# Kernel optimization log

Hardware: AMD Instinct MI355X
Metric: run time of the kernel (lower is better)

Reference implementation:

```python
import jax, jax.numpy as jnp
import numpy as np

B, S, D, H = 2, 2048, 1024, 16
HEAD_DIM = D // H
SCALE = HEAD_DIM ** -0.5


def setup_inputs() -> dict:
    key = jax.random.key(0)
    k1, k2, k3 = jax.random.split(key, 3)
    x = jax.random.normal(k1, (B, S, D), dtype=jnp.float32)
    # torch nn.Linear convention: weight is [out_features, in_features], y = x @ W.T + b
    W_qkv = jax.random.normal(k2, (3 * D, D), dtype=jnp.float32) * 0.02  # qkv Linear, bias=False
    W_out = jax.random.normal(k3, (D, D), dtype=jnp.float32) * 0.02
    b_out = jnp.zeros((D,), dtype=jnp.float32)
    return {"x": x, "W_qkv": W_qkv, "W_out": W_out, "b_out": b_out}


def reference(x, W_qkv, W_out, b_out):
    b, s, d_model = x.shape
    # qkv projection (no bias), then split 'b c (qkv h d) -> qkv b h c d'
    qkv = (x @ W_qkv.T).reshape(b, s, 3, H, HEAD_DIM).transpose(2, 0, 3, 1, 4)
    q, k, v = qkv[0], qkv[1], qkv[2]  # each [b, h, s, hd]
    # naive full attention: scores materialized as [b, h, s, s]
    attn = jax.nn.softmax(jnp.einsum('bhxd,bhyd->bhxy', q, k) * SCALE, axis=-1)
    # dropout is identity (rate 0 / eval mode)
    o = jnp.einsum('bhxy,bhyd->bhxd', attn, v)
    o = o.transpose(0, 2, 1, 3).reshape(b, s, d_model)  # 'b h c d -> b c (h d)'
    return o @ W_out.T + b_out
```

## Files before the change

### kernel.cpp

```cpp
#include <hip/hip_runtime.h>


typedef __attribute__((ext_vector_type(8))) short short8;
typedef __attribute__((ext_vector_type(4))) float f32x4;
typedef unsigned short ushort_t;
typedef unsigned int uint32;

#define AS1 __attribute__((address_space(1)))
#define AS3 __attribute__((address_space(3)))

__device__ __forceinline__ void gload_lds16(const void* gp, void* lp) {
    __builtin_amdgcn_global_load_lds((const AS1 void*)gp, (AS3 void*)lp, 16, 0, 0);
}

#if __has_builtin(__builtin_amdgcn_exp2f)
#define EXP2F(x) __builtin_amdgcn_exp2f(x)
#else
#define EXP2F(x) exp2f(x)
#endif

__device__ __forceinline__ uint32 rhu(float f) { return __float_as_uint(f) + 0x8000u; }
#if __has_builtin(__builtin_amdgcn_perm)
__device__ __forceinline__ uint32 pk2bf(float a, float b) {
    return __builtin_amdgcn_perm(rhu(b), rhu(a), 0x07060302u);
}
#else
__device__ __forceinline__ uint32 pk2bf(float a, float b) {
    return (rhu(a) >> 16) | (rhu(b) & 0xffff0000u);
}
#endif
__device__ __forceinline__ ushort_t f2bf(float f) { return (ushort_t)(rhu(f) >> 16); }

__global__ void cvt_all(const float* __restrict__ x, ushort_t* __restrict__ xb,
                        const float* __restrict__ wq, ushort_t* __restrict__ wqb,
                        const float* __restrict__ wo, ushort_t* __restrict__ wob) {
    int blk = blockIdx.x;
    const float* in; ushort_t* out;
    if (blk < 4096)      { in = x;  out = xb;  }
    else if (blk < 7168) { in = wq; out = wqb; blk -= 4096; }
    else                 { in = wo; out = wob; blk -= 7168; }
    const int i = (blk * 256 + threadIdx.x) * 4;
    const float4 v = *(const float4*)(in + i);
    uint2 pk;
    pk.x = pk2bf(v.x, v.y);
    pk.y = pk2bf(v.z, v.w);
    *(uint2*)(out + i) = pk;
}

__global__ __launch_bounds__(256, 2)
void gemm_bt_bf16(const ushort_t* __restrict__ A, const ushort_t* __restrict__ B,
                  ushort_t* __restrict__ Cb, float* __restrict__ Cf,
                  const float* __restrict__ bias, ushort_t* __restrict__ vT,
                  int M, int N, int K, int ldc, float qScale) {
    __shared__ ushort_t lA[128 * 32];
    __shared__ ushort_t lB[128 * 32];
    const int tid = threadIdx.x;
    const int wave = tid >> 6, lane = tid & 63;
    const int quad = lane >> 4, l16 = lane & 15;
    const int wr = wave >> 1, wc = wave & 1;
    const int mBase = blockIdx.y * 128, nBase = blockIdx.x * 128;

    f32x4 acc[4][4];
#pragma unroll
    for (int i = 0; i < 4; i++)
#pragma unroll
        for (int j = 0; j < 4; j++) acc[i][j] = (f32x4){0.f, 0.f, 0.f, 0.f};

    const int ar = tid >> 2;
    const int ac = (((tid & 3) ^ ((ar >> 1) & 3)) * 8);
    const int rsw = ((l16 >> 1) & 3);

    const ushort_t* aptr = A + (size_t)(mBase + ar) * K + ac;
    const ushort_t* bptr = B + (size_t)(nBase + ar) * K + ac;

    for (int k0 = 0; k0 < K; k0 += 32) {
#pragma unroll
        for (int c = 0; c < 2; c++) {
            gload_lds16(aptr + (size_t)(c * 64) * K + k0, lA + c * 2048 + wave * 512);
            gload_lds16(bptr + (size_t)(c * 64) * K + k0, lB + c * 2048 + wave * 512);
        }
        __syncthreads();

        short8 af[4], bf[4];
#pragma unroll
        for (int i = 0; i < 4; i++)
            af[i] = *(const short8*)(lA + (wr * 64 + i * 16 + l16) * 32 + ((quad ^ rsw) * 8));
#pragma unroll
        for (int j = 0; j < 4; j++)
            bf[j] = *(const short8*)(lB + (wc * 64 + j * 16 + l16) * 32 + ((quad ^ rsw) * 8));
#pragma unroll
        for (int i = 0; i < 4; i++)
#pragma unroll
            for (int j = 0; j < 4; j++)
                acc[i][j] = __builtin_amdgcn_mfma_f32_16x16x32_bf16(af[i], bf[j], acc[i][j], 0, 0, 0);
        __syncthreads();
    }

    if (vT && nBase >= 2048) {
#pragma unroll
        for (int i = 0; i < 4; i++)
#pragma unroll
            for (int j = 0; j < 4; j++) {
                const int row0 = mBase + wr * 64 + i * 16 + quad * 4;
                const int col = nBase + wc * 64 + j * 16 + l16 - 2048;
                const int b = row0 >> 11, s0 = row0 & 2047;
                uint2 pk;
                pk.x = pk2bf(acc[i][j][0], acc[i][j][1]);
                pk.y = pk2bf(acc[i][j][2], acc[i][j][3]);
                *(uint2*)(vT + ((size_t)(b * 16) * 64 + col) * 2048 + s0) = pk;
            }
        return;
    }
    const float cs = (vT && nBase < 1024) ? qScale : 1.0f;
#pragma unroll
    for (int i = 0; i < 4; i++)
#pragma unroll
        for (int j = 0; j < 4; j++)
#pragma unroll
            for (int r = 0; r < 4; r++) {
                const int row = mBase + wr * 64 + i * 16 + quad * 4 + r;
                const int col = nBase + wc * 64 + j * 16 + l16;
                const float v = acc[i][j][r];
                if (Cb) Cb[(size_t)row * ldc + col] = f2bf(v * cs);
                else    Cf[(size_t)row * ldc + col] = v + bias[col];
            }
}

__global__ __launch_bounds__(256, 4)
void attn_flash(const ushort_t* __restrict__ qk, const ushort_t* __restrict__ vT,
                ushort_t* __restrict__ o) {
    __shared__ ushort_t lK[128 * 64];
    __shared__ ushort_t lV[64 * 128];
    __shared__ ushort_t lP[4][16 * 40];

    const int tid = threadIdx.x;
    const int wave = tid >> 6, lane = tid & 63;
    const int quad = lane >> 4, l16 = lane & 15;
    const int bh = blockIdx.y;
    const int b = bh >> 4, h = bh & 15;
    const size_t rowBase = (size_t)b * 2048;
    const int qCol = h * 64, kCol = 1024 + h * 64;
    const int qRow0 = blockIdx.x * 64;
    const int swz = (l16 & 7);

    const int sr = tid >> 3;
    const int sc = ((tid & 7) ^ (sr & 7)) * 8;
    const int vr = tid >> 4;
    const int vc = ((tid & 15) ^ (vr & 7)) * 8;

#pragma unroll
    for (int cc = 0; cc < 2; cc++)
        gload_lds16(qk + (rowBase + qRow0 + cc * 32 + sr) * 2048 + qCol + sc,
                    lK + cc * 2048 + wave * 512);
    __syncthreads();
    short8 qf[2];
#pragma unroll
    for (int ks = 0; ks < 2; ks++)
        qf[ks] = *(const short8*)(lK + (wave * 16 + l16) * 64 + (((ks * 4 + quad) ^ swz) * 8));
    __syncthreads();

    short8 onesA;
#pragma unroll
    for (int i = 0; i < 8; i++) onesA[i] = (short)0x3F80;

    f32x4 oacc[4];
    f32x4 lacc = (f32x4){0.f, 0.f, 0.f, 0.f};
#pragma unroll
    for (int dt = 0; dt < 4; dt++) oacc[dt] = (f32x4){0.f, 0.f, 0.f, 0.f};

    const ushort_t* kptr = qk + (rowBase + sr) * 2048 + kCol + sc;
    const ushort_t* vptr = vT + ((size_t)bh * 64 + vr) * 2048 + vc;

    for (int kt = 0; kt < 16; kt++) {
#pragma unroll
        for (int cc = 0; cc < 4; cc++)
            gload_lds16(kptr + (size_t)(cc * 32) * 2048, lK + cc * 2048 + wave * 512);
#pragma unroll
        for (int cc = 0; cc < 4; cc++)
            gload_lds16(vptr + (size_t)(cc * 16) * 2048, lV + cc * 2048 + wave * 512);
        kptr += 128 * 2048;
        vptr += 128;
        __syncthreads();

        f32x4 sacc[8];
#pragma unroll
        for (int mt = 0; mt < 8; mt++) {
            const short8 k0 = *(const short8*)(lK + (mt * 16 + l16) * 64 + ((quad ^ swz) * 8));
            const short8 k1 = *(const short8*)(lK + (mt * 16 + l16) * 64 + (((4 + quad) ^ swz) * 8));
            f32x4 t = (f32x4){0.f, 0.f, 0.f, 0.f};
            t = __builtin_amdgcn_mfma_f32_16x16x32_bf16(k0, qf[0], t, 0, 0, 0);
            t = __builtin_amdgcn_mfma_f32_16x16x32_bf16(k1, qf[1], t, 0, 0, 0);
            sacc[mt] = t;
        }

#pragma unroll
        for (int kk = 0; kk < 4; kk++) {
#pragma unroll
            for (int t16 = 0; t16 < 2; t16++) {
                const f32x4 s = sacc[2 * kk + t16];
                uint2 pk;
                pk.x = pk2bf(EXP2F(s[0]), EXP2F(s[1]));
                pk.y = pk2bf(EXP2F(s[2]), EXP2F(s[3]));
                *(uint2*)(&lP[wave][l16 * 40 + t16 * 16 + quad * 4]) = pk;
            }
            const short8 pf = *(const short8*)(&lP[wave][l16 * 40 + quad * 8]);
            lacc = __builtin_amdgcn_mfma_f32_16x16x32_bf16(onesA, pf, lacc, 0, 0, 0);
#pragma unroll
            for (int dt = 0; dt < 4; dt++) {
                const short8 vf = *(const short8*)(lV + (dt * 16 + l16) * 128 +
                                                   (((kk * 4 + quad) ^ swz) * 8));
                oacc[dt] = __builtin_amdgcn_mfma_f32_16x16x32_bf16(vf, pf, oacc[dt], 0, 0, 0);
            }
        }
        __syncthreads();
    }

    const float inv = 1.0f / lacc[0];
    const size_t row = rowBase + qRow0 + wave * 16 + l16;
#pragma unroll
    for (int dt = 0; dt < 4; dt++) {
        uint2 pk;
        pk.x = pk2bf(oacc[dt][0] * inv, oacc[dt][1] * inv);
        pk.y = pk2bf(oacc[dt][2] * inv, oacc[dt][3] * inv);
        *(uint2*)(o + row * 1024 + h * 64 + dt * 16 + quad * 4) = pk;
    }
}

extern "C" void kernel_launch(void* const* d_in, const int* in_sizes, int n_in,
                              void* d_out, int out_size, void* d_ws, size_t ws_size,
                              hipStream_t stream) {
    const float* x    = (const float*)d_in[0];
    const float* Wqkv = (const float*)d_in[1];
    const float* Wout = (const float*)d_in[2];
    const float* bout = (const float*)d_in[3];
    float* out = (float*)d_out;

    ushort_t* xb    = (ushort_t*)d_ws;
    ushort_t* wqkvb = xb + (size_t)4096 * 1024;
    ushort_t* woutb = wqkvb + (size_t)3072 * 1024;
    ushort_t* qkb   = woutb + (size_t)1024 * 1024;
    ushort_t* vTb   = qkb + (size_t)4096 * 2048;
    ushort_t* ob    = xb;

    const float SC = 0.125f * 1.44269504089f;

    cvt_all<<<8192, 256, 0, stream>>>(x, xb, Wqkv, wqkvb, Wout, woutb);
    gemm_bt_bf16<<<dim3(24, 32), 256, 0, stream>>>(xb, wqkvb, qkb, nullptr, nullptr, vTb,
                                                   4096, 3072, 1024, 2048, SC);
    attn_flash<<<dim3(32, 32), 256, 0, stream>>>(qkb, vTb, ob);
    gemm_bt_bf16<<<dim3(8, 32), 256, 0, stream>>>(ob, woutb, nullptr, out, bout, nullptr,
                                                  4096, 1024, 1024, 1024, 1.0f);
}
```

Before: 199.0 us.

## Double-buffer LDS tiles in GEMMs and attention, retile output projection

Adds double-buffered LDS staging to the QKV GEMM, the attention kernel and a new output-projection GEMM. Each kernel now prefetches the next tile while computing the current one, and one barrier per iteration replaces two. Attention uses 64-key tiles instead of 128, which keeps LDS usage roughly constant while doubling the buffer count. The output GEMM is split into its own kernel with 64x128 tiles and K-step 64, launching twice as many blocks to fill the CUs, at the cost of more instantiated kernels and higher LDS use per block.

```diff
diff --git a/kernel.cpp b/kernel.cpp
--- a/kernel.cpp
+++ b/kernel.cpp
@@ -48,12 +48,11 @@
 }
 
 __global__ __launch_bounds__(256, 2)
-void gemm_bt_bf16(const ushort_t* __restrict__ A, const ushort_t* __restrict__ B,
-                  ushort_t* __restrict__ Cb, float* __restrict__ Cf,
-                  const float* __restrict__ bias, ushort_t* __restrict__ vT,
-                  int M, int N, int K, int ldc, float qScale) {
-    __shared__ ushort_t lA[128 * 32];
-    __shared__ ushort_t lB[128 * 32];
+void gemm_qkv(const ushort_t* __restrict__ A, const ushort_t* __restrict__ B,
+              ushort_t* __restrict__ Cb, ushort_t* __restrict__ vT,
+              int M, int N, int K, int ldc, float qScale) {
+    __shared__ ushort_t lA[2][128 * 32];
+    __shared__ ushort_t lB[2][128 * 32];
     const int tid = threadIdx.x;
     const int wave = tid >> 6, lane = tid & 63;
     const int quad = lane >> 4, l16 = lane & 15;
@@ -73,30 +72,35 @@
     const ushort_t* aptr = A + (size_t)(mBase + ar) * K + ac;
     const ushort_t* bptr = B + (size_t)(nBase + ar) * K + ac;
 
+#define G1_STAGE(buf, k0)                                                            \
+    {                                                                                \
+        _Pragma("unroll") for (int c = 0; c < 2; c++) {                              \
+            gload_lds16(aptr + (size_t)(c * 64) * K + (k0), lA[buf] + c * 2048 + wave * 512); \
+            gload_lds16(bptr + (size_t)(c * 64) * K + (k0), lB[buf] + c * 2048 + wave * 512); \
+        }                                                                            \
+    }
+
+    G1_STAGE(0, 0);
     for (int k0 = 0; k0 < K; k0 += 32) {
-#pragma unroll
-        for (int c = 0; c < 2; c++) {
-            gload_lds16(aptr + (size_t)(c * 64) * K + k0, lA + c * 2048 + wave * 512);
-            gload_lds16(bptr + (size_t)(c * 64) * K + k0, lB + c * 2048 + wave * 512);
-        }
+        const int cur = (k0 >> 5) & 1;
         __syncthreads();
+        if (k0 + 32 < K) G1_STAGE(cur ^ 1, k0 + 32);
 
         short8 af[4], bf[4];
 #pragma unroll
         for (int i = 0; i < 4; i++)
-            af[i] = *(const short8*)(lA + (wr * 64 + i * 16 + l16) * 32 + ((quad ^ rsw) * 8));
+            af[i] = *(const short8*)(lA[cur] + (wr * 64 + i * 16 + l16) * 32 + ((quad ^ rsw) * 8));
 #pragma unroll
         for (int j = 0; j < 4; j++)
-            bf[j] = *(const short8*)(lB + (wc * 64 + j * 16 + l16) * 32 + ((quad ^ rsw) * 8));
+            bf[j] = *(const short8*)(lB[cur] + (wc * 64 + j * 16 + l16) * 32 + ((quad ^ rsw) * 8));
 #pragma unroll
         for (int i = 0; i < 4; i++)
 #pragma unroll
             for (int j = 0; j < 4; j++)
                 acc[i][j] = __builtin_amdgcn_mfma_f32_16x16x32_bf16(af[i], bf[j], acc[i][j], 0, 0, 0);
-        __syncthreads();
-    }
-
-    if (vT && nBase >= 2048) {
+    }
+
+    if (nBase >= 2048) {
 #pragma unroll
         for (int i = 0; i < 4; i++)
 #pragma unroll
@@ -111,7 +115,7 @@
             }
         return;
     }
-    const float cs = (vT && nBase < 1024) ? qScale : 1.0f;
+    const float cs = (nBase < 1024) ? qScale : 1.0f;
 #pragma unroll
     for (int i = 0; i < 4; i++)
 #pragma unroll
@@ -120,17 +124,82 @@
             for (int r = 0; r < 4; r++) {
                 const int row = mBase + wr * 64 + i * 16 + quad * 4 + r;
                 const int col = nBase + wc * 64 + j * 16 + l16;
-                const float v = acc[i][j][r];
-                if (Cb) Cb[(size_t)row * ldc + col] = f2bf(v * cs);
-                else    Cf[(size_t)row * ldc + col] = v + bias[col];
+                Cb[(size_t)row * ldc + col] = f2bf(acc[i][j][r] * cs);
+            }
+}
+
+__global__ __launch_bounds__(256, 2)
+void gemm_out(const ushort_t* __restrict__ A, const ushort_t* __restrict__ B,
+              float* __restrict__ Cf, const float* __restrict__ bias,
+              int M, int N, int K) {
+    __shared__ ushort_t lA[2][64 * 64];
+    __shared__ ushort_t lB[2][128 * 64];
+    const int tid = threadIdx.x;
+    const int wave = tid >> 6, lane = tid & 63;
+    const int quad = lane >> 4, l16 = lane & 15;
+    const int mBase = blockIdx.y * 64, nBase = blockIdx.x * 128;
+
+    f32x4 acc[4][2];
+#pragma unroll
+    for (int i = 0; i < 4; i++)
+#pragma unroll
+        for (int j = 0; j < 2; j++) acc[i][j] = (f32x4){0.f, 0.f, 0.f, 0.f};
+
+    const int sr = tid >> 3;
+    const int sc = ((tid & 7) ^ (sr & 7)) * 8;
+    const int swz = l16 & 7;
+
+    const ushort_t* aptr = A + (size_t)(mBase + sr) * K + sc;
+    const ushort_t* bptr = B + (size_t)(nBase + sr) * K + sc;
+
+#define G2_STAGE(buf, k0)                                                              \
+    {                                                                                  \
+        _Pragma("unroll") for (int c = 0; c < 2; c++)                                  \
+            gload_lds16(aptr + (size_t)(c * 32) * K + (k0), lA[buf] + c * 2048 + wave * 512); \
+        _Pragma("unroll") for (int c = 0; c < 4; c++)                                  \
+            gload_lds16(bptr + (size_t)(c * 32) * K + (k0), lB[buf] + c * 2048 + wave * 512); \
+    }
+
+    G2_STAGE(0, 0);
+    for (int k0 = 0; k0 < K; k0 += 64) {
+        const int cur = (k0 >> 6) & 1;
+        __syncthreads();
+        if (k0 + 64 < K) G2_STAGE(cur ^ 1, k0 + 64);
+
+#pragma unroll
+        for (int ks = 0; ks < 2; ks++) {
+            short8 af[4], bf[2];
+#pragma unroll
+            for (int i = 0; i < 4; i++)
+                af[i] = *(const short8*)(lA[cur] + (i * 16 + l16) * 64 + (((ks * 4 + quad) ^ swz) * 8));
+#pragma unroll
+            for (int j = 0; j < 2; j++)
+                bf[j] = *(const short8*)(lB[cur] + (wave * 32 + j * 16 + l16) * 64 + (((ks * 4 + quad) ^ swz) * 8));
+#pragma unroll
+            for (int i = 0; i < 4; i++)
+#pragma unroll
+                for (int j = 0; j < 2; j++)
+                    acc[i][j] = __builtin_amdgcn_mfma_f32_16x16x32_bf16(af[i], bf[j], acc[i][j], 0, 0, 0);
+        }
+    }
+
+#pragma unroll
+    for (int i = 0; i < 4; i++)
+#pragma unroll
+        for (int j = 0; j < 2; j++)
+#pragma unroll
+            for (int r = 0; r < 4; r++) {
+                const int row = mBase + i * 16 + quad * 4 + r;
+                const int col = nBase + wave * 32 + j * 16 + l16;
+                Cf[(size_t)row * N + col] = acc[i][j][r] + bias[col];
             }
 }
 
 __global__ __launch_bounds__(256, 4)
 void attn_flash(const ushort_t* __restrict__ qk, const ushort_t* __restrict__ vT,
                 ushort_t* __restrict__ o) {
-    __shared__ ushort_t lK[128 * 64];
-    __shared__ ushort_t lV[64 * 128];
+    __shared__ ushort_t lK[2][64 * 64];
+    __shared__ ushort_t lV[2][64 * 64];
     __shared__ ushort_t lP[4][16 * 40];
 
     const int tid = threadIdx.x;
@@ -141,22 +210,20 @@
     const size_t rowBase = (size_t)b * 2048;
     const int qCol = h * 64, kCol = 1024 + h * 64;
     const int qRow0 = blockIdx.x * 64;
-    const int swz = (l16 & 7);
+    const int swz = l16 & 7;
 
     const int sr = tid >> 3;
     const int sc = ((tid & 7) ^ (sr & 7)) * 8;
-    const int vr = tid >> 4;
-    const int vc = ((tid & 15) ^ (vr & 7)) * 8;
 
 #pragma unroll
     for (int cc = 0; cc < 2; cc++)
         gload_lds16(qk + (rowBase + qRow0 + cc * 32 + sr) * 2048 + qCol + sc,
-                    lK + cc * 2048 + wave * 512);
+                    lK[0] + cc * 2048 + wave * 512);
     __syncthreads();
     short8 qf[2];
 #pragma unroll
     for (int ks = 0; ks < 2; ks++)
-        qf[ks] = *(const short8*)(lK + (wave * 16 + l16) * 64 + (((ks * 4 + quad) ^ swz) * 8));
+        qf[ks] = *(const short8*)(lK[0] + (wave * 16 + l16) * 64 + (((ks * 4 + quad) ^ swz) * 8));
     __syncthreads();
 
     short8 onesA;
@@ -169,24 +236,27 @@
     for (int dt = 0; dt < 4; dt++) oacc[dt] = (f32x4){0.f, 0.f, 0.f, 0.f};
 
     const ushort_t* kptr = qk + (rowBase + sr) * 2048 + kCol + sc;
-    const ushort_t* vptr = vT + ((size_t)bh * 64 + vr) * 2048 + vc;
-
-    for (int kt = 0; kt < 16; kt++) {
-#pragma unroll
-        for (int cc = 0; cc < 4; cc++)
-            gload_lds16(kptr + (size_t)(cc * 32) * 2048, lK + cc * 2048 + wave * 512);
-#pragma unroll
-        for (int cc = 0; cc < 4; cc++)
-            gload_lds16(vptr + (size_t)(cc * 16) * 2048, lV + cc * 2048 + wave * 512);
-        kptr += 128 * 2048;
-        vptr += 128;
+    const ushort_t* vptr = vT + ((size_t)bh * 64 + sr) * 2048 + sc;
+
+#define AT_STAGE(buf, kt)                                                                 \
+    {                                                                                     \
+        _Pragma("unroll") for (int cc = 0; cc < 2; cc++)                                  \
+            gload_lds16(kptr + (size_t)((kt) * 64 + cc * 32) * 2048, lK[buf] + cc * 2048 + wave * 512); \
+        _Pragma("unroll") for (int cc = 0; cc < 2; cc++)                                  \
+            gload_lds16(vptr + (size_t)(cc * 32) * 2048 + (kt) * 64, lV[buf] + cc * 2048 + wave * 512); \
+    }
+
+    AT_STAGE(0, 0);
+    for (int kt = 0; kt < 32; kt++) {
+        const int cur = kt & 1;
         __syncthreads();
-
-        f32x4 sacc[8];
-#pragma unroll
-        for (int mt = 0; mt < 8; mt++) {
-            const short8 k0 = *(const short8*)(lK + (mt * 16 + l16) * 64 + ((quad ^ swz) * 8));
-            const short8 k1 = *(const short8*)(lK + (mt * 16 + l16) * 64 + (((4 + quad) ^ swz) * 8));
+        if (kt < 31) AT_STAGE(cur ^ 1, kt + 1);
+
+        f32x4 sacc[4];
+#pragma unroll
+        for (int mt = 0; mt < 4; mt++) {
+            const short8 k0 = *(const short8*)(lK[cur] + (mt * 16 + l16) * 64 + ((quad ^ swz) * 8));
+            const short8 k1 = *(const short8*)(lK[cur] + (mt * 16 + l16) * 64 + (((4 + quad) ^ swz) * 8));
             f32x4 t = (f32x4){0.f, 0.f, 0.f, 0.f};
             t = __builtin_amdgcn_mfma_f32_16x16x32_bf16(k0, qf[0], t, 0, 0, 0);
             t = __builtin_amdgcn_mfma_f32_16x16x32_bf16(k1, qf[1], t, 0, 0, 0);
@@ -194,7 +264,7 @@
         }
 
 #pragma unroll
-        for (int kk = 0; kk < 4; kk++) {
+        for (int kk = 0; kk < 2; kk++) {
 #pragma unroll
             for (int t16 = 0; t16 < 2; t16++) {
                 const f32x4 s = sacc[2 * kk + t16];
@@ -207,12 +277,11 @@
             lacc = __builtin_amdgcn_mfma_f32_16x16x32_bf16(onesA, pf, lacc, 0, 0, 0);
 #pragma unroll
             for (int dt = 0; dt < 4; dt++) {
-                const short8 vf = *(const short8*)(lV + (dt * 16 + l16) * 128 +
+                const short8 vf = *(const short8*)(lV[cur] + (dt * 16 + l16) * 64 +
                                                    (((kk * 4 + quad) ^ swz) * 8));
                 oacc[dt] = __builtin_amdgcn_mfma_f32_16x16x32_bf16(vf, pf, oacc[dt], 0, 0, 0);
             }
         }
-        __syncthreads();
     }
 
     const float inv = 1.0f / lacc[0];
@@ -245,9 +314,7 @@
     const float SC = 0.125f * 1.44269504089f;
 
     cvt_all<<<8192, 256, 0, stream>>>(x, xb, Wqkv, wqkvb, Wout, woutb);
-    gemm_bt_bf16<<<dim3(24, 32), 256, 0, stream>>>(xb, wqkvb, qkb, nullptr, nullptr, vTb,
-                                                   4096, 3072, 1024, 2048, SC);
+    gemm_qkv<<<dim3(24, 32), 256, 0, stream>>>(xb, wqkvb, qkb, vTb, 4096, 3072, 1024, 2048, SC);
     attn_flash<<<dim3(32, 32), 256, 0, stream>>>(qkb, vTb, ob);
-    gemm_bt_bf16<<<dim3(8, 32), 256, 0, stream>>>(ob, woutb, nullptr, out, bout, nullptr,
-                                                  4096, 1024, 1024, 1024, 1.0f);
-}
+    gemm_out<<<dim3(8, 64), 256, 0, stream>>>(ob, woutb, out, bout, 4096, 1024, 1024);
+}
```

Result: faster. 186.6 us (-6.2%).
